# Kernel tuning notes

Hardware: AMD Instinct MI355X
Metric: run time of the kernel (lower is better)

## Reference

```python
import jax, jax.numpy as jnp
import numpy as np

BATCH, HIDDEN, DIM_X, N_FORCING, DIM_T, MODES = 16, 128, 128, 4, 64, 96


def setup_inputs() -> dict:
    key = jax.random.key(0)
    k1, k2, k3, k4, k5 = jax.random.split(key, 5)
    scale = 1.0 / HIDDEN ** 2
    return {
        "z0": jax.random.normal(k1, (BATCH, HIDDEN, DIM_X), jnp.float32),
        "xi": jax.random.normal(k2, (BATCH, N_FORCING, DIM_X, DIM_T), jnp.float32),
        "A": scale * jax.random.uniform(k3, (2, MODES, HIDDEN, HIDDEN), jnp.float32),
        "W_F": jax.random.normal(k4, (HIDDEN, HIDDEN), jnp.float32) / np.sqrt(HIDDEN).astype(np.float32),
        "W_G": jax.random.normal(k5, (HIDDEN, N_FORCING, HIDDEN), jnp.float32) / np.sqrt(HIDDEN).astype(np.float32),
    }


def _spde_func(z, W_F, W_G):
    # z: (b, h, x) -> F_z: (b, h, x), G_z: (b, h, n, x)
    F_z = jnp.tanh(jnp.einsum('oh,bhx->box', W_F, z))
    G_z = jnp.tanh(jnp.einsum('onh,bhx->bonx', W_G, z))
    return F_z, G_z


def _compl_mat_vec_mul_1d(A, z):
    # A: (2, modes, h, h); z: (batch, 2, modes, h) -- (real, imag) stacked on dim 1
    op = lambda M, u: jnp.einsum('xij,bxj->bxi', M, u)
    re = op(A[0], z[:, 0]) - op(A[1], z[:, 1])
    im = op(A[1], z[:, 0]) - op(A[0], z[:, 1])  # faithful to original (minus sign)
    return jnp.stack([re, im], axis=1)


def _prod(v, xi_t, A, W_F, W_G, a, b):
    # v: (batch, 2, dim_x, hidden); xi_t: (batch, dim_x, n_forcing) = dX/dt at step i
    Av = jnp.zeros_like(v).at[:, :, a:b].set(_compl_mat_vec_mul_1d(A, v[:, :, a:b]))
    vc = v[:, 0] + 1j * v[:, 1]                      # (b, x, h) complex
    z = jnp.fft.ifft(jnp.fft.ifftshift(vc, axes=1), axis=1).real  # (b, x, h)
    z = jnp.transpose(z, (0, 2, 1))                  # (b, h, x)
    F_z, G_z = _spde_func(z, W_F, W_G)
    G_z_xi = jnp.einsum('bhnx,bxn->bhx', G_z, xi_t)
    H = F_z + G_z_xi                                 # (b, h, x)
    hf = jnp.fft.fftshift(jnp.fft.fft(H, axis=2), axes=2)
    hf = jnp.stack([hf.real, hf.imag], axis=1)       # (b, 2, h, x)
    hf = jnp.transpose(hf, (0, 1, 3, 2))             # (b, 2, x, h)
    out_ft = jnp.zeros_like(v).at[:, :, a:b].set(hf[:, :, a:b])
    return Av + out_ft


def reference(z0, xi, A, W_F, W_G):
    batch, hidden, dim_x = z0.shape
    modes = A.shape[1]
    a, b = dim_x // 2 - modes // 2, dim_x // 2 + modes // 2
    # v0: band-limited shifted FFT of z0, layout (b, 2, x, h)
    z0_ft = jnp.fft.fftshift(jnp.fft.fft(z0, axis=2), axes=2)
    z0_ft = jnp.stack([z0_ft.real, z0_ft.imag], axis=1)            # (b, 2, h, x)
    v0 = jnp.zeros_like(z0_ft).at[:, :, :, a:b].set(z0_ft[:, :, :, a:b])
    v0 = jnp.transpose(v0, (0, 1, 3, 2))                           # (b, 2, x, h)
    # control increments: linear interp slope on uniform grid t=arange(T), dt=1
    xi_path = jnp.transpose(xi, (0, 2, 3, 1))                      # (b, x, t, n)
    dxi = xi_path[:, :, 1:, :] - xi_path[:, :, :-1, :]             # (b, x, t-1, n)
    dxi = jnp.moveaxis(dxi, 2, 0)                                  # (t-1, b, x, n)

    def step(v, d):
        v_new = v + _prod(v, d, A, W_F, W_G, a, b)  # Euler, dt = 1
        return v_new, v_new

    _, traj = jax.lax.scan(step, v0, dxi)                          # (t-1, b, 2, x, h)
    traj = jnp.concatenate([v0[None], traj], axis=0)               # (t, b, 2, x, h)
    vc = traj[:, :, 0] + 1j * traj[:, :, 1]                        # (t, b, x, h)
    vc = jnp.transpose(vc, (1, 3, 2, 0))                           # (b, h, x, t)
    z = jnp.fft.ifft(jnp.fft.ifftshift(vc, axes=2), axis=2).real   # (b, h, x, t)
    return z
```

## Files before the change

kernel.cpp:

```cpp
#include <hip/hip_runtime.h>
#include <math.h>

#define BATCH 16
#define HID   128
#define NX    128
#define NF    4
#define NT    64
#define MODES 96
#define OM    (5 * HID)
#define MATS  ((size_t)BATCH * HID * NX)

__global__ void k_tables(float* __restrict__ C, float* __restrict__ S,
                         float2* __restrict__ T2) {
    int m = blockIdx.x;
    int x = threadIdx.x;
    if (x < NX) {
        int k = (80 + m) % NX;
        float ang = (float)((k * x) & (NX - 1)) * (2.0f * (float)M_PI / (float)NX);
        float c = cosf(ang), s = sinf(ang);
        C[m * NX + x] = c;
        S[m * NX + x] = s;
        T2[m * NX + x] = make_float2(c, s);
    }
}

__global__ void k_dxi(const float* __restrict__ xi, float* __restrict__ dxi) {
    int idx = blockIdx.x * blockDim.x + threadIdx.x;
    const int total = (NT - 1) * BATCH * NX * NF;
    if (idx < total) {
        int n = idx & (NF - 1);
        int x = (idx >> 2) & (NX - 1);
        int b = (idx >> 9) & (BATCH - 1);
        int t = idx >> 13;
        const float* base = xi + (((size_t)b * NF + n) * NX + x) * NT;
        dxi[idx] = base[t + 1] - base[t];
    }
}

__global__ void k_wt(const float* __restrict__ WF, const float* __restrict__ WG,
                     float* __restrict__ Wt) {
    __shared__ float t[32][33];
    int g = blockIdx.z;
    int h0 = blockIdx.x * 32, o0 = blockIdx.y * 32;
    int tx = threadIdx.x, ty = threadIdx.y;
    #pragma unroll
    for (int j = 0; j < 32; j += 8) {
        int o = o0 + ty + j;
        t[ty + j][tx] = (g == 0) ? WF[(size_t)o * HID + h0 + tx]
                                 : WG[((size_t)o * NF + (g - 1)) * HID + h0 + tx];
    }
    __syncthreads();
    #pragma unroll
    for (int j = 0; j < 32; j += 8)
        Wt[(size_t)(h0 + ty + j) * OM + g * HID + o0 + tx] = t[tx][ty + j];
}

__global__ void k_at2(const float* __restrict__ A, float2* __restrict__ At2) {
    __shared__ float t0[32][33], t1[32][33];
    int m = blockIdx.z;
    int h0 = blockIdx.x * 32, o0 = blockIdx.y * 32;
    int tx = threadIdx.x, ty = threadIdx.y;
    const float* A0 = A + (size_t)m * HID * HID;
    const float* A1 = A0 + (size_t)MODES * HID * HID;
    #pragma unroll
    for (int j = 0; j < 32; j += 8) {
        t0[ty + j][tx] = A0[(size_t)(o0 + ty + j) * HID + h0 + tx];
        t1[ty + j][tx] = A1[(size_t)(o0 + ty + j) * HID + h0 + tx];
    }
    __syncthreads();
    #pragma unroll
    for (int j = 0; j < 32; j += 8)
        At2[((size_t)m * HID + h0 + ty + j) * HID + o0 + tx] =
            make_float2(t0[tx][ty + j], t1[tx][ty + j]);
}

__global__ __launch_bounds__(256) void k_v0(const float* __restrict__ z0,
                                            const float* __restrict__ C,
                                            const float* __restrict__ S,
                                            float* __restrict__ v) {
    int m = blockIdx.x, b = blockIdx.y;
    int h = threadIdx.x & 127;
    int c = threadIdx.x >> 7;
    const float* zr = z0 + ((size_t)b * HID + h) * NX;
    const float* T  = (c == 0) ? (C + m * NX) : (S + m * NX);
    float acc = 0.f;
    for (int x = 0; x < NX; ++x) acc += zr[x] * T[x];
    if (c) acc = -acc;
    v[(((size_t)b * 2 + c) * MODES + m) * HID + h] = acc;
}

__global__ __launch_bounds__(512) void k_step1a(
    const float* __restrict__ v, const float* __restrict__ Ct,
    const float* __restrict__ St, float* __restrict__ zstep,
    float* __restrict__ out, int step, int zdirect)
{
    __shared__ float Cs[MODES][8], Ss[MODES][8];
    int xt = blockIdx.x, b = blockIdx.y;
    int tid = threadIdx.x;
    int xg0 = xt * 8;
    for (int i = tid; i < MODES * 8; i += 512) {
        int m = i >> 3, xl = i & 7;
        Cs[m][xl] = Ct[m * NX + xg0 + xl];
        Ss[m][xl] = St[m * NX + xg0 + xl];
    }
    __syncthreads();
    int h = tid & 127, xp = tid >> 7;
    int xl0 = xp * 2;
    const float* vr = v + ((size_t)b * 2) * MODES * HID + h;
    const float* vi = vr + (size_t)MODES * HID;
    float a0 = 0.f, a1 = 0.f;
    #pragma unroll 8
    for (int m = 0; m < MODES; ++m) {
        float r  = vr[m * HID];
        float im = vi[m * HID];
        a0 += r * Cs[m][xl0]     - im * Ss[m][xl0];
        a1 += r * Cs[m][xl0 + 1] - im * Ss[m][xl0 + 1];
    }
    const float inv = 1.0f / (float)NX;
    a0 *= inv; a1 *= inv;
    size_t zb = (((size_t)b * NX + xg0 + xl0) * HID) + h;
    zstep[zb] = a0;
    zstep[zb + HID] = a1;
    if (zdirect) {
        size_t ob = (((size_t)b * HID + h) * NX + xg0 + xl0) * NT + step;
        out[ob] = a0; out[ob + NT] = a1;
    }
}

__global__ __launch_bounds__(256) void k_step1b(
    const float* __restrict__ zsrc, const float* __restrict__ Wt,
    float* __restrict__ Hp)
{
    __shared__ float zs[32][132];
    int bx0 = blockIdx.x * 32;
    int om0 = blockIdx.y * 64;
    int tid = threadIdx.x;
    const float4* z4 = (const float4*)zsrc;
    #pragma unroll
    for (int p = 0; p < 4; ++p) {
        int idx = tid + p * 256;
        int row = idx >> 5, c4 = idx & 31;
        float4 zv = z4[(size_t)(bx0 + row) * 32 + c4];
        *((float4*)&zs[row][c4 * 4]) = zv;
    }
    __syncthreads();
    int bxt = tid & 15, ot = tid >> 4;
    const float4* W4 = (const float4*)Wt;
    int wcol = (om0 >> 2) + ot;
    float a00=0,a01=0,a10=0,a11=0,a20=0,a21=0,a30=0,a31=0;
    #pragma unroll 4
    for (int h = 0; h < HID; ++h) {
        float4 w = W4[(size_t)h * (OM / 4) + wcol];
        float z0v = zs[bxt][h];
        float z1v = zs[bxt + 16][h];
        a00 += w.x * z0v; a01 += w.x * z1v;
        a10 += w.y * z0v; a11 += w.y * z1v;
        a20 += w.z * z0v; a21 += w.z * z1v;
        a30 += w.w * z0v; a31 += w.w * z1v;
    }
    int b = bx0 >> 7, x0 = bx0 & 127;
    float r0[4] = {a00, a10, a20, a30};
    float r1[4] = {a01, a11, a21, a31};
    #pragma unroll
    for (int j = 0; j < 4; ++j) {
        int om = om0 + ot * 4 + j;
        int mat = om >> 7, o = om & 127;
        size_t base = (((size_t)mat * BATCH + b) * HID + o) * NX + x0;
        Hp[base + bxt]      = r0[j];
        Hp[base + bxt + 16] = r1[j];
    }
}

__global__ __launch_bounds__(128) void k_step2a(
    const float* __restrict__ Hp, const float2* __restrict__ T2g,
    const float* __restrict__ dxi, float* __restrict__ hf, int step)
{
    __shared__ float Hcl[8][132];
    __shared__ float Csh[32][140];
    __shared__ float Ssh[32][140];
    __shared__ float red[4][32][16];
    int b = blockIdx.x, og = blockIdx.y, mg = blockIdx.z;
    int tid = threadIdx.x;

    for (int p = 0; p < 32; ++p) {
        int idx = tid + p * 128;
        int mm = idx >> 7, x = idx & 127;
        float2 t = T2g[(size_t)(mg * 32 + mm) * NX + x];
        Csh[mm][x] = t.x;
        Ssh[mm][x] = t.y;
    }
    {
        int x = tid;
        const float4* dx4p = (const float4*)(dxi + (((size_t)step * BATCH + b) * NX + x) * NF);
        float4 dx = dx4p[0];
        const float* hp = Hp + ((size_t)b * HID + og * 8) * NX + x;
        #pragma unroll
        for (int o = 0; o < 8; ++o) {
            const float* p = hp + (size_t)o * NX;
            float f  = tanhf(p[0]);
            float g0 = tanhf(p[MATS]);
            float g1 = tanhf(p[2 * MATS]);
            float g2 = tanhf(p[3 * MATS]);
            float g3 = tanhf(p[4 * MATS]);
            Hcl[o][x] = f + g0 * dx.x + g1 * dx.y + g2 * dx.z + g3 * dx.w;
        }
    }
    __syncthreads();

    int othr = tid & 1, mthr = (tid >> 1) & 15, xh = tid >> 5;
    int x0 = xh * 32;
    float re[4][2] = {}, im[4][2] = {};
    for (int i = 0; i < 32; i += 4) {
        float4 hc0 = *(const float4*)&Hcl[othr * 4 + 0][x0 + i];
        float4 hc1 = *(const float4*)&Hcl[othr * 4 + 1][x0 + i];
        float4 hc2 = *(const float4*)&Hcl[othr * 4 + 2][x0 + i];
        float4 hc3 = *(const float4*)&Hcl[othr * 4 + 3][x0 + i];
        #pragma unroll
        for (int mI = 0; mI < 2; ++mI) {
            float4 c4 = *(const float4*)&Csh[mthr * 2 + mI][x0 + i];
            float4 s4 = *(const float4*)&Ssh[mthr * 2 + mI][x0 + i];
            re[0][mI] += hc0.x*c4.x + hc0.y*c4.y + hc0.z*c4.z + hc0.w*c4.w;
            im[0][mI] -= hc0.x*s4.x + hc0.y*s4.y + hc0.z*s4.z + hc0.w*s4.w;
            re[1][mI] += hc1.x*c4.x + hc1.y*c4.y + hc1.z*c4.z + hc1.w*c4.w;
            im[1][mI] -= hc1.x*s4.x + hc1.y*s4.y + hc1.z*s4.z + hc1.w*s4.w;
            re[2][mI] += hc2.x*c4.x + hc2.y*c4.y + hc2.z*c4.z + hc2.w*c4.w;
            im[2][mI] -= hc2.x*s4.x + hc2.y*s4.y + hc2.z*s4.z + hc2.w*s4.w;
            re[3][mI] += hc3.x*c4.x + hc3.y*c4.y + hc3.z*c4.z + hc3.w*c4.w;
            im[3][mI] -= hc3.x*s4.x + hc3.y*s4.y + hc3.z*s4.z + hc3.w*s4.w;
        }
    }
    int slot = othr + 2 * mthr;
    #pragma unroll
    for (int oI = 0; oI < 4; ++oI)
        #pragma unroll
        for (int mI = 0; mI < 2; ++mI) {
            red[xh][slot][(oI * 2 + mI) * 2 + 0] = re[oI][mI];
            red[xh][slot][(oI * 2 + mI) * 2 + 1] = im[oI][mI];
        }
    __syncthreads();
    #pragma unroll
    for (int q = 0; q < 4; ++q) {
        int u = tid + q * 128;
        int o_l = u & 7, m_l = (u >> 3) & 31, ri = u >> 8;
        int so = o_l >> 2, oI = o_l & 3, sm = m_l >> 1, mI = m_l & 1;
        int sl = so + 2 * sm;
        int vv = (oI * 2 + mI) * 2 + ri;
        float sum = red[0][sl][vv] + red[1][sl][vv] + red[2][sl][vv] + red[3][sl][vv];
        hf[(((size_t)ri * MODES + mg * 32 + m_l) * BATCH + b) * HID + og * 8 + o_l] = sum;
    }
}

__global__ __launch_bounds__(256) void k_step2b(
    const float* __restrict__ vin, const float2* __restrict__ At2,
    const float* __restrict__ hf, float* __restrict__ vout)
{
    __shared__ float2 vs2[8][HID];
    int oq = blockIdx.x, bp = blockIdx.y, m = blockIdx.z;
    int tid = threadIdx.x;
    for (int idx = tid; idx < 8 * HID; idx += 256) {
        int bb = idx >> 7, h = idx & 127;
        size_t base = (((size_t)(bp * 8 + bb) * 2) * MODES + m) * HID + h;
        vs2[bb][h] = make_float2(vin[base], vin[base + (size_t)MODES * HID]);
    }
    __syncthreads();
    int o = oq * 32 + (tid & 31);
    int bl = tid >> 5;
    int b = bp * 8 + bl;
    const float2* a2 = At2 + (size_t)m * HID * HID + o;
    float are = 0.f, aim = 0.f;
    #pragma unroll 4
    for (int h = 0; h < HID; ++h) {
        float2 a = a2[(size_t)h * HID];
        float2 vv = vs2[bl][h];
        are += a.x * vv.x - a.y * vv.y;
        aim += a.y * vv.x - a.x * vv.y;
    }
    float fre = hf[((size_t)m * BATCH + b) * HID + o];
    float fim = hf[(((size_t)MODES + m) * BATCH + b) * HID + o];
    float2 vo = vs2[bl][o];
    size_t ob = (((size_t)b * 2) * MODES + m) * HID + o;
    vout[ob] = vo.x + are + fre;
    vout[ob + (size_t)MODES * HID] = vo.y + aim + fim;
}

__global__ __launch_bounds__(256) void k_flush(const float* __restrict__ zbuf,
                                               float* __restrict__ out, int t0) {
    int x = blockIdx.x, b = blockIdx.y, tid = threadIdx.x;
    __shared__ float tile[16][HID];
    for (int i = tid; i < 16 * HID; i += 256) {
        int tt = i >> 7, h = i & 127;
        tile[tt][h] = zbuf[(((size_t)tt * BATCH + b) * NX + x) * HID + h];
    }
    __syncthreads();
    int h = tid >> 1, half = tid & 1;
    float4 w[2];
    float* wp = (float*)w;
    #pragma unroll
    for (int j = 0; j < 8; ++j) wp[j] = tile[half * 8 + j][h];
    float4* dst = (float4*)(out + (((size_t)b * HID + h) * NX + x) * NT + t0 + half * 8);
    dst[0] = w[0];
    dst[1] = w[1];
}

extern "C" void kernel_launch(void* const* d_in, const int* in_sizes, int n_in,
                              void* d_out, int out_size, void* d_ws, size_t ws_size,
                              hipStream_t stream) {
    const float* z0 = (const float*)d_in[0];
    const float* xi = (const float*)d_in[1];
    const float* A  = (const float*)d_in[2];
    const float* WF = (const float*)d_in[3];
    const float* WG = (const float*)d_in[4];
    float* out = (float*)d_out;

    float* ws = (float*)d_ws;
    size_t cap = ws_size / sizeof(float);
    size_t off = 0;
    auto alloc = [&](size_t n) { float* p = ws + off; off += n; return p; };

    float*  Ct   = alloc((size_t)MODES * NX);
    float*  St   = alloc((size_t)MODES * NX);
    float2* T2g  = (float2*)alloc((size_t)MODES * NX * 2);
    float*  Wt   = alloc((size_t)HID * OM);
    float2* At2  = (float2*)alloc((size_t)MODES * HID * HID * 2);
    float*  v0b  = alloc((size_t)BATCH * 2 * MODES * HID);
    float*  v1b  = alloc((size_t)BATCH * 2 * MODES * HID);
    float*  Hp   = alloc((size_t)5 * BATCH * HID * NX);
    float*  hfb  = alloc((size_t)2 * MODES * BATCH * HID);
    float*  dxib = alloc((size_t)(NT - 1) * BATCH * NX * NF);

    const size_t ZSZ = (size_t)BATCH * NX * HID;
    float* zbuf = nullptr;
    if (off + 16 * ZSZ <= cap) zbuf = alloc(16 * ZSZ);
    float* zsingle = nullptr;
    if (!zbuf) zsingle = alloc(ZSZ);
    int zdirect = (zbuf == nullptr) ? 1 : 0;

    k_tables<<<MODES, 128, 0, stream>>>(Ct, St, T2g);
    {
        int total = (NT - 1) * BATCH * NX * NF;
        k_dxi<<<(total + 255) / 256, 256, 0, stream>>>(xi, dxib);
    }
    k_wt<<<dim3(4, 4, 5), dim3(32, 8), 0, stream>>>(WF, WG, Wt);
    k_at2<<<dim3(4, 4, MODES), dim3(32, 8), 0, stream>>>(A, At2);
    k_v0<<<dim3(MODES, BATCH), 256, 0, stream>>>(z0, Ct, St, v0b);

    float* vcur = v0b;
    float* vnxt = v1b;
    for (int i = 0; i < NT - 1; ++i) {
        float* zstep = zdirect ? zsingle : (zbuf + (size_t)(i & 15) * ZSZ);
        k_step1a<<<dim3(16, BATCH), 512, 0, stream>>>(vcur, Ct, St, zstep, out, i, zdirect);
        k_step1b<<<dim3(64, 10), 256, 0, stream>>>(zstep, Wt, Hp);
        k_step2a<<<dim3(BATCH, 16, 3), 128, 0, stream>>>(Hp, T2g, dxib, hfb, i);
        k_step2b<<<dim3(4, 2, MODES), 256, 0, stream>>>(vcur, At2, hfb, vnxt);
        float* t = vcur; vcur = vnxt; vnxt = t;
        if (!zdirect && (i & 15) == 15)
            k_flush<<<dim3(NX, BATCH), 256, 0, stream>>>(zbuf, out, i - 15);
    }
    {
        float* zstep = zdirect ? zsingle : (zbuf + (size_t)((NT - 1) & 15) * ZSZ);
        k_step1a<<<dim3(16, BATCH), 512, 0, stream>>>(vcur, Ct, St, zstep, out, NT - 1, zdirect);
        if (!zdirect)
            k_flush<<<dim3(NX, BATCH), 256, 0, stream>>>(zbuf, out, NT - 16);
    }
}
```

Measured before the change: 3.702 ms.

## Fuse per-step pipeline from four kernels into two with in-kernel projection and DFT

Each Euler step drops from four launches to two. k_s1 does the inverse DFT to z, the W_F/W_G projection, tanh and the forcing contraction in shared memory, and writes only the combined H. k_s2 folds the forward DFT of H into the spectral mat-vec kernel. This removes the 5-matrix Hp round trip, the hf buffer and two launches per step. In exchange, the forward DFT is recomputed in every (batch-pair, mode) block, k_s1 has only 256 blocks doing serial 128-long projection loops, and W is re-read per block.

```diff
diff --git a/kernel.cpp b/kernel.cpp
--- a/kernel.cpp
+++ b/kernel.cpp
@@ -8,7 +8,7 @@
 #define NT    64
 #define MODES 96
 #define OM    (5 * HID)
-#define MATS  ((size_t)BATCH * HID * NX)
+#define XT1   8
 
 __global__ void k_tables(float* __restrict__ C, float* __restrict__ S,
                          float2* __restrict__ T2) {
@@ -89,194 +89,161 @@
     v[(((size_t)b * 2 + c) * MODES + m) * HID + h] = acc;
 }
 
-__global__ __launch_bounds__(512) void k_step1a(
+__global__ __launch_bounds__(512) void k_s1(
     const float* __restrict__ v, const float* __restrict__ Ct,
-    const float* __restrict__ St, float* __restrict__ zstep,
-    float* __restrict__ out, int step, int zdirect)
+    const float* __restrict__ St, const float* __restrict__ Wt,
+    const float* __restrict__ dxi, float* __restrict__ Hc,
+    float* __restrict__ zstep, float* __restrict__ out,
+    int step, int writeH, int zdirect)
 {
-    __shared__ float Cs[MODES][8], Ss[MODES][8];
+    __shared__ float Cs[MODES][XT1];
+    __shared__ float Ss[MODES][XT1];
+    __shared__ float zs[HID][XT1];
+    __shared__ float Ht[5][HID][XT1];
+    __shared__ float dxs[XT1][NF];
     int xt = blockIdx.x, b = blockIdx.y;
     int tid = threadIdx.x;
-    int xg0 = xt * 8;
-    for (int i = tid; i < MODES * 8; i += 512) {
+    int xg0 = xt * XT1;
+
+    for (int i = tid; i < MODES * XT1; i += 512) {
         int m = i >> 3, xl = i & 7;
         Cs[m][xl] = Ct[m * NX + xg0 + xl];
         Ss[m][xl] = St[m * NX + xg0 + xl];
     }
-    __syncthreads();
-    int h = tid & 127, xp = tid >> 7;
-    int xl0 = xp * 2;
-    const float* vr = v + ((size_t)b * 2) * MODES * HID + h;
-    const float* vi = vr + (size_t)MODES * HID;
-    float a0 = 0.f, a1 = 0.f;
-    #pragma unroll 8
-    for (int m = 0; m < MODES; ++m) {
-        float r  = vr[m * HID];
-        float im = vi[m * HID];
-        a0 += r * Cs[m][xl0]     - im * Ss[m][xl0];
-        a1 += r * Cs[m][xl0 + 1] - im * Ss[m][xl0 + 1];
-    }
-    const float inv = 1.0f / (float)NX;
-    a0 *= inv; a1 *= inv;
-    size_t zb = (((size_t)b * NX + xg0 + xl0) * HID) + h;
-    zstep[zb] = a0;
-    zstep[zb + HID] = a1;
-    if (zdirect) {
-        size_t ob = (((size_t)b * HID + h) * NX + xg0 + xl0) * NT + step;
-        out[ob] = a0; out[ob + NT] = a1;
-    }
-}
-
-__global__ __launch_bounds__(256) void k_step1b(
-    const float* __restrict__ zsrc, const float* __restrict__ Wt,
-    float* __restrict__ Hp)
+    if (writeH && tid < XT1 * NF) {
+        int xl = tid >> 2, n = tid & 3;
+        dxs[xl][n] = dxi[(((size_t)step * BATCH + b) * NX + xg0 + xl) * NF + n];
+    }
+    __syncthreads();
+
+    {
+        int h = tid & 127, xp = tid >> 7;
+        int x0 = xp * 2;
+        const float* vr = v + ((size_t)b * 2) * MODES * HID + h;
+        const float* vi = vr + (size_t)MODES * HID;
+        float a0 = 0.f, a1 = 0.f;
+        #pragma unroll 4
+        for (int m = 0; m < MODES; ++m) {
+            float r  = vr[m * HID];
+            float im = vi[m * HID];
+            float2 c2 = *(const float2*)&Cs[m][x0];
+            float2 s2 = *(const float2*)&Ss[m][x0];
+            a0 += r * c2.x - im * s2.x;
+            a1 += r * c2.y - im * s2.y;
+        }
+        const float inv = 1.0f / (float)NX;
+        a0 *= inv; a1 *= inv;
+        *(float2*)&zs[h][x0] = make_float2(a0, a1);
+        size_t zb = ((size_t)b * NX + xg0 + x0) * HID + h;
+        zstep[zb] = a0;
+        zstep[zb + HID] = a1;
+        if (zdirect) {
+            size_t ob = (((size_t)b * HID + h) * NX + xg0 + x0) * NT + step;
+            out[ob] = a0; out[ob + NT] = a1;
+        }
+    }
+    __syncthreads();
+    if (!writeH) return;
+
+    {
+        float acc0[XT1] = {0,0,0,0,0,0,0,0};
+        float acc1[XT1] = {0,0,0,0,0,0,0,0};
+        const float* w0 = Wt + tid;
+        const float* w1 = Wt + 512 + (tid & 127);
+        bool rep1 = (tid < 128);
+        #pragma unroll 2
+        for (int h = 0; h < HID; ++h) {
+            float4 za = *(const float4*)&zs[h][0];
+            float4 zb4 = *(const float4*)&zs[h][4];
+            float w = w0[(size_t)h * OM];
+            acc0[0] += w * za.x;  acc0[1] += w * za.y;
+            acc0[2] += w * za.z;  acc0[3] += w * za.w;
+            acc0[4] += w * zb4.x; acc0[5] += w * zb4.y;
+            acc0[6] += w * zb4.z; acc0[7] += w * zb4.w;
+            if (rep1) {
+                float w2 = w1[(size_t)h * OM];
+                acc1[0] += w2 * za.x;  acc1[1] += w2 * za.y;
+                acc1[2] += w2 * za.z;  acc1[3] += w2 * za.w;
+                acc1[4] += w2 * zb4.x; acc1[5] += w2 * zb4.y;
+                acc1[6] += w2 * zb4.z; acc1[7] += w2 * zb4.w;
+            }
+        }
+        {
+            int g = tid >> 7, o = tid & 127;
+            float4 t0 = make_float4(tanhf(acc0[0]), tanhf(acc0[1]),
+                                    tanhf(acc0[2]), tanhf(acc0[3]));
+            float4 t1 = make_float4(tanhf(acc0[4]), tanhf(acc0[5]),
+                                    tanhf(acc0[6]), tanhf(acc0[7]));
+            *(float4*)&Ht[g][o][0] = t0;
+            *(float4*)&Ht[g][o][4] = t1;
+        }
+        if (rep1) {
+            int o = tid & 127;
+            float4 t0 = make_float4(tanhf(acc1[0]), tanhf(acc1[1]),
+                                    tanhf(acc1[2]), tanhf(acc1[3]));
+            float4 t1 = make_float4(tanhf(acc1[4]), tanhf(acc1[5]),
+                                    tanhf(acc1[6]), tanhf(acc1[7]));
+            *(float4*)&Ht[4][o][0] = t0;
+            *(float4*)&Ht[4][o][4] = t1;
+        }
+    }
+    __syncthreads();
+
+    {
+        int o = tid & 127, xh = tid >> 7;
+        #pragma unroll
+        for (int j = 0; j < 2; ++j) {
+            int x = xh * 2 + j;
+            float hv = Ht[0][o][x];
+            #pragma unroll
+            for (int n = 0; n < NF; ++n)
+                hv += Ht[1 + n][o][x] * dxs[x][n];
+            Hc[((size_t)b * NX + xg0 + x) * HID + o] = hv;
+        }
+    }
+}
+
+__global__ __launch_bounds__(256) void k_s2(
+    const float* __restrict__ vin, const float2* __restrict__ At2,
+    const float2* __restrict__ T2g, const float* __restrict__ Hc,
+    float* __restrict__ vout)
 {
-    __shared__ float zs[32][132];
-    int bx0 = blockIdx.x * 32;
-    int om0 = blockIdx.y * 64;
+    __shared__ float2 vs2[2][HID];
+    __shared__ float2 T2s[NX];
+    int bq = blockIdx.x, m = blockIdx.y;
     int tid = threadIdx.x;
-    const float4* z4 = (const float4*)zsrc;
-    #pragma unroll
-    for (int p = 0; p < 4; ++p) {
-        int idx = tid + p * 256;
-        int row = idx >> 5, c4 = idx & 31;
-        float4 zv = z4[(size_t)(bx0 + row) * 32 + c4];
-        *((float4*)&zs[row][c4 * 4]) = zv;
-    }
-    __syncthreads();
-    int bxt = tid & 15, ot = tid >> 4;
-    const float4* W4 = (const float4*)Wt;
-    int wcol = (om0 >> 2) + ot;
-    float a00=0,a01=0,a10=0,a11=0,a20=0,a21=0,a30=0,a31=0;
+    int b0 = bq * 2;
+    if (tid < NX) T2s[tid] = T2g[(size_t)m * NX + tid];
+    if (tid >= NX) {
+        int idx = tid - NX;
+        int bl = idx >> 6, hh = (idx & 63) * 2;
+        size_t base = (((size_t)(b0 + bl) * 2) * MODES + m) * HID + hh;
+        size_t imo = (size_t)MODES * HID;
+        vs2[bl][hh]     = make_float2(vin[base],     vin[base + imo]);
+        vs2[bl][hh + 1] = make_float2(vin[base + 1], vin[base + 1 + imo]);
+    }
+    __syncthreads();
+    int o = tid & 127, bl = tid >> 7;
+    int b = b0 + bl;
+
+    const float* hp = Hc + (size_t)b * NX * HID + o;
+    float fre = 0.f, fim = 0.f;
     #pragma unroll 4
-    for (int h = 0; h < HID; ++h) {
-        float4 w = W4[(size_t)h * (OM / 4) + wcol];
-        float z0v = zs[bxt][h];
-        float z1v = zs[bxt + 16][h];
-        a00 += w.x * z0v; a01 += w.x * z1v;
-        a10 += w.y * z0v; a11 += w.y * z1v;
-        a20 += w.z * z0v; a21 += w.z * z1v;
-        a30 += w.w * z0v; a31 += w.w * z1v;
-    }
-    int b = bx0 >> 7, x0 = bx0 & 127;
-    float r0[4] = {a00, a10, a20, a30};
-    float r1[4] = {a01, a11, a21, a31};
-    #pragma unroll
-    for (int j = 0; j < 4; ++j) {
-        int om = om0 + ot * 4 + j;
-        int mat = om >> 7, o = om & 127;
-        size_t base = (((size_t)mat * BATCH + b) * HID + o) * NX + x0;
-        Hp[base + bxt]      = r0[j];
-        Hp[base + bxt + 16] = r1[j];
-    }
-}
-
-__global__ __launch_bounds__(128) void k_step2a(
-    const float* __restrict__ Hp, const float2* __restrict__ T2g,
-    const float* __restrict__ dxi, float* __restrict__ hf, int step)
-{
-    __shared__ float Hcl[8][132];
-    __shared__ float Csh[32][140];
-    __shared__ float Ssh[32][140];
-    __shared__ float red[4][32][16];
-    int b = blockIdx.x, og = blockIdx.y, mg = blockIdx.z;
-    int tid = threadIdx.x;
-
-    for (int p = 0; p < 32; ++p) {
-        int idx = tid + p * 128;
-        int mm = idx >> 7, x = idx & 127;
-        float2 t = T2g[(size_t)(mg * 32 + mm) * NX + x];
-        Csh[mm][x] = t.x;
-        Ssh[mm][x] = t.y;
-    }
-    {
-        int x = tid;
-        const float4* dx4p = (const float4*)(dxi + (((size_t)step * BATCH + b) * NX + x) * NF);
-        float4 dx = dx4p[0];
-        const float* hp = Hp + ((size_t)b * HID + og * 8) * NX + x;
-        #pragma unroll
-        for (int o = 0; o < 8; ++o) {
-            const float* p = hp + (size_t)o * NX;
-            float f  = tanhf(p[0]);
-            float g0 = tanhf(p[MATS]);
-            float g1 = tanhf(p[2 * MATS]);
-            float g2 = tanhf(p[3 * MATS]);
-            float g3 = tanhf(p[4 * MATS]);
-            Hcl[o][x] = f + g0 * dx.x + g1 * dx.y + g2 * dx.z + g3 * dx.w;
-        }
-    }
-    __syncthreads();
-
-    int othr = tid & 1, mthr = (tid >> 1) & 15, xh = tid >> 5;
-    int x0 = xh * 32;
-    float re[4][2] = {}, im[4][2] = {};
-    for (int i = 0; i < 32; i += 4) {
-        float4 hc0 = *(const float4*)&Hcl[othr * 4 + 0][x0 + i];
-        float4 hc1 = *(const float4*)&Hcl[othr * 4 + 1][x0 + i];
-        float4 hc2 = *(const float4*)&Hcl[othr * 4 + 2][x0 + i];
-        float4 hc3 = *(const float4*)&Hcl[othr * 4 + 3][x0 + i];
-        #pragma unroll
-        for (int mI = 0; mI < 2; ++mI) {
-            float4 c4 = *(const float4*)&Csh[mthr * 2 + mI][x0 + i];
-            float4 s4 = *(const float4*)&Ssh[mthr * 2 + mI][x0 + i];
-            re[0][mI] += hc0.x*c4.x + hc0.y*c4.y + hc0.z*c4.z + hc0.w*c4.w;
-            im[0][mI] -= hc0.x*s4.x + hc0.y*s4.y + hc0.z*s4.z + hc0.w*s4.w;
-            re[1][mI] += hc1.x*c4.x + hc1.y*c4.y + hc1.z*c4.z + hc1.w*c4.w;
-            im[1][mI] -= hc1.x*s4.x + hc1.y*s4.y + hc1.z*s4.z + hc1.w*s4.w;
-            re[2][mI] += hc2.x*c4.x + hc2.y*c4.y + hc2.z*c4.z + hc2.w*c4.w;
-            im[2][mI] -= hc2.x*s4.x + hc2.y*s4.y + hc2.z*s4.z + hc2.w*s4.w;
-            re[3][mI] += hc3.x*c4.x + hc3.y*c4.y + hc3.z*c4.z + hc3.w*c4.w;
-            im[3][mI] -= hc3.x*s4.x + hc3.y*s4.y + hc3.z*s4.z + hc3.w*s4.w;
-        }
-    }
-    int slot = othr + 2 * mthr;
-    #pragma unroll
-    for (int oI = 0; oI < 4; ++oI)
-        #pragma unroll
-        for (int mI = 0; mI < 2; ++mI) {
-            red[xh][slot][(oI * 2 + mI) * 2 + 0] = re[oI][mI];
-            red[xh][slot][(oI * 2 + mI) * 2 + 1] = im[oI][mI];
-        }
-    __syncthreads();
-    #pragma unroll
-    for (int q = 0; q < 4; ++q) {
-        int u = tid + q * 128;
-        int o_l = u & 7, m_l = (u >> 3) & 31, ri = u >> 8;
-        int so = o_l >> 2, oI = o_l & 3, sm = m_l >> 1, mI = m_l & 1;
-        int sl = so + 2 * sm;
-        int vv = (oI * 2 + mI) * 2 + ri;
-        float sum = red[0][sl][vv] + red[1][sl][vv] + red[2][sl][vv] + red[3][sl][vv];
-        hf[(((size_t)ri * MODES + mg * 32 + m_l) * BATCH + b) * HID + og * 8 + o_l] = sum;
-    }
-}
-
-__global__ __launch_bounds__(256) void k_step2b(
-    const float* __restrict__ vin, const float2* __restrict__ At2,
-    const float* __restrict__ hf, float* __restrict__ vout)
-{
-    __shared__ float2 vs2[8][HID];
-    int oq = blockIdx.x, bp = blockIdx.y, m = blockIdx.z;
-    int tid = threadIdx.x;
-    for (int idx = tid; idx < 8 * HID; idx += 256) {
-        int bb = idx >> 7, h = idx & 127;
-        size_t base = (((size_t)(bp * 8 + bb) * 2) * MODES + m) * HID + h;
-        vs2[bb][h] = make_float2(vin[base], vin[base + (size_t)MODES * HID]);
-    }
-    __syncthreads();
-    int o = oq * 32 + (tid & 31);
-    int bl = tid >> 5;
-    int b = bp * 8 + bl;
+    for (int x = 0; x < NX; ++x) {
+        float hv = hp[(size_t)x * HID];
+        float2 t = T2s[x];
+        fre += hv * t.x;
+        fim -= hv * t.y;
+    }
     const float2* a2 = At2 + (size_t)m * HID * HID + o;
     float are = 0.f, aim = 0.f;
     #pragma unroll 4
     for (int h = 0; h < HID; ++h) {
-        float2 a = a2[(size_t)h * HID];
+        float2 a  = a2[(size_t)h * HID];
         float2 vv = vs2[bl][h];
         are += a.x * vv.x - a.y * vv.y;
         aim += a.y * vv.x - a.x * vv.y;
     }
-    float fre = hf[((size_t)m * BATCH + b) * HID + o];
-    float fim = hf[(((size_t)MODES + m) * BATCH + b) * HID + o];
     float2 vo = vs2[bl][o];
     size_t ob = (((size_t)b * 2) * MODES + m) * HID + o;
     vout[ob] = vo.x + are + fre;
@@ -324,8 +291,7 @@
     float2* At2  = (float2*)alloc((size_t)MODES * HID * HID * 2);
     float*  v0b  = alloc((size_t)BATCH * 2 * MODES * HID);
     float*  v1b  = alloc((size_t)BATCH * 2 * MODES * HID);
-    float*  Hp   = alloc((size_t)5 * BATCH * HID * NX);
-    float*  hfb  = alloc((size_t)2 * MODES * BATCH * HID);
+    float*  Hcb  = alloc((size_t)BATCH * NX * HID);
     float*  dxib = alloc((size_t)(NT - 1) * BATCH * NX * NF);
 
     const size_t ZSZ = (size_t)BATCH * NX * HID;
@@ -348,17 +314,17 @@
     float* vnxt = v1b;
     for (int i = 0; i < NT - 1; ++i) {
         float* zstep = zdirect ? zsingle : (zbuf + (size_t)(i & 15) * ZSZ);
-        k_step1a<<<dim3(16, BATCH), 512, 0, stream>>>(vcur, Ct, St, zstep, out, i, zdirect);
-        k_step1b<<<dim3(64, 10), 256, 0, stream>>>(zstep, Wt, Hp);
-        k_step2a<<<dim3(BATCH, 16, 3), 128, 0, stream>>>(Hp, T2g, dxib, hfb, i);
-        k_step2b<<<dim3(4, 2, MODES), 256, 0, stream>>>(vcur, At2, hfb, vnxt);
+        k_s1<<<dim3(NX / XT1, BATCH), 512, 0, stream>>>(
+            vcur, Ct, St, Wt, dxib, Hcb, zstep, out, i, 1, zdirect);
+        k_s2<<<dim3(8, MODES), 256, 0, stream>>>(vcur, At2, T2g, Hcb, vnxt);
         float* t = vcur; vcur = vnxt; vnxt = t;
         if (!zdirect && (i & 15) == 15)
             k_flush<<<dim3(NX, BATCH), 256, 0, stream>>>(zbuf, out, i - 15);
     }
     {
         float* zstep = zdirect ? zsingle : (zbuf + (size_t)((NT - 1) & 15) * ZSZ);
-        k_step1a<<<dim3(16, BATCH), 512, 0, stream>>>(vcur, Ct, St, zstep, out, NT - 1, zdirect);
+        k_s1<<<dim3(NX / XT1, BATCH), 512, 0, stream>>>(
+            vcur, Ct, St, Wt, dxib, Hcb, zstep, out, NT - 1, 0, zdirect);
         if (!zdirect)
             k_flush<<<dim3(NX, BATCH), 256, 0, stream>>>(zbuf, out, NT - 16);
     }
```

After: 4.761 ms. 1.29x slower.
